# Kernel optimization log

Measured on AMD Instinct MI355X. Metric: run time of the kernel, lower is better.

Reference implementation:

```python
import jax, jax.numpy as jnp
import numpy as np

HIDDEN = 1024
B, S = 4, 2048


def setup_inputs() -> dict:
    key = jax.random.key(0)
    ks = jax.random.split(key, 9)
    scale = 1.0 / np.sqrt(HIDDEN)
    mk = lambda k: (jax.random.normal(k, (HIDDEN, HIDDEN), dtype=jnp.float32) * scale)
    return {
        "x": jax.random.normal(ks[0], (B, S, HIDDEN), dtype=jnp.float32),
        "Wq": mk(ks[1]), "bq": jnp.zeros((HIDDEN,), jnp.float32),
        "Wk": mk(ks[2]), "bk": jnp.zeros((HIDDEN,), jnp.float32),
        "Wv": mk(ks[3]), "bv": jnp.zeros((HIDDEN,), jnp.float32),
        "Wo": mk(ks[4]), "bo": jnp.zeros((HIDDEN,), jnp.float32),
    }


def reference(x, Wq, bq, Wk, bk, Wv, bv, Wo, bo):
    # Single-head attention over the full hidden dim (num_heads unused in source).
    # Linear(H,H): y = x @ W^T + b ; weights stored [out,in] torch-style.
    q = jnp.einsum("bsh,oh->bso", x, Wq) + bq  # [B,S,H]
    k = jnp.einsum("bsh,oh->bso", x, Wk) + bk
    v = jnp.einsum("bsh,oh->bso", x, Wv) + bv
    scores = jnp.einsum("bqh,bkh->bqk", q, k) / jnp.sqrt(jnp.float32(HIDDEN))
    attn = jax.nn.softmax(scores, axis=-1)  # dropout rate is 0.0 (eval-equivalent)
    ctx = jnp.einsum("bqk,bkh->bqh", attn, v)
    return jnp.einsum("bsh,oh->bso", ctx, Wo) + bo
```

## Files before the change

kernel.cpp:

```cpp
#include <hip/hip_runtime.h>

#define HID 1024
#define SEQ 2048
#define NB 4
#define BS 8192

typedef __attribute__((ext_vector_type(8))) short short8;
typedef __attribute__((ext_vector_type(8))) unsigned short ushort8;
typedef __attribute__((ext_vector_type(4))) float f32x4;

__device__ __forceinline__ float bf2f(unsigned short u) {
  unsigned int x = ((unsigned int)u) << 16;
  return __builtin_bit_cast(float, x);
}
__device__ __forceinline__ unsigned short f2bf(float f) {
  unsigned int x = __builtin_bit_cast(unsigned int, f);
  x = x + 0x7fffu + ((x >> 16) & 1u);
  return (unsigned short)(x >> 16);
}

#define GLOAD16(g, l)                                                          \
  __builtin_amdgcn_global_load_lds(                                            \
      (const __attribute__((address_space(1))) unsigned int*)(g),              \
      (__attribute__((address_space(3))) unsigned int*)(l), 16, 0, 0)

__global__ void cast_f32_to_bf16(const float* __restrict__ in,
                                 unsigned short* __restrict__ out, int n) {
  int i = (blockIdx.x * 256 + threadIdx.x) * 8;
  if (i >= n) return;
  f32x4 a = *(const f32x4*)(in + i);
  f32x4 b = *(const f32x4*)(in + i + 4);
  ushort8 o;
  o[0] = f2bf(a[0]); o[1] = f2bf(a[1]); o[2] = f2bf(a[2]); o[3] = f2bf(a[3]);
  o[4] = f2bf(b[0]); o[5] = f2bf(b[1]); o[6] = f2bf(b[2]); o[7] = f2bf(b[3]);
  *(ushort8*)(out + i) = o;
}

__global__ __launch_bounds__(256) void transpose_cast(
    const float* __restrict__ in, unsigned short* __restrict__ out) {
  __shared__ float t[32][33];
  const int bx = blockIdx.x * 32, by = blockIdx.y * 32;
  const int tx = threadIdx.x & 31, ty = threadIdx.x >> 5;
#pragma unroll
  for (int i = 0; i < 4; ++i)
    t[ty + i * 8][tx] = in[(by + ty + i * 8) * 1024 + bx + tx];
  __syncthreads();
#pragma unroll
  for (int i = 0; i < 4; ++i)
    out[(bx + ty + i * 8) * 1024 + by + tx] = f2bf(t[tx][ty + i * 8]);
}

__global__ __launch_bounds__(256) void bias_fuse(const float* __restrict__ Wo,
                                                 const float* __restrict__ bv,
                                                 const float* __restrict__ bo,
                                                 float* __restrict__ bp) {
  const int row = blockIdx.x * 4 + (threadIdx.x >> 6);
  const int lane = threadIdx.x & 63;
  float s = 0.f;
  for (int k = lane; k < 1024; k += 64) s += Wo[row * 1024 + k] * bv[k];
#pragma unroll
  for (int off = 32; off >= 1; off >>= 1) s += __shfl_xor(s, off, 64);
  if (lane == 0) bp[row] = s + bo[row];
}

template <int BN, int OUT_F32, int BIAS_MODE, int EPI>
__global__ __launch_bounds__(512, 2) void gemm2p(
    const unsigned short* __restrict__ A, const unsigned short* __restrict__ B,
    void* __restrict__ Cv, const float* __restrict__ bias,
    const float* __restrict__ bias2, float* __restrict__ Srow, int K, int lda,
    int ldb, int ldc, long long bsA, long long bsB, long long bsC,
    float alpha) {
  static_assert(BN == 256 || BN == 128, "BN");
  constexpr int WMW = (BN == 256) ? 2 : 4;
  constexpr int WNW = 8 / WMW;
  constexpr int MI = (256 / WMW) / 16;
  constexpr int GB = BN / 64;
  constexpr int WROWS = 256 / WMW;

  __shared__ unsigned short lA[2][256 * 64];
  __shared__ unsigned short lB[2][BN * 64];

  const int tid = threadIdx.x;
  const int lane = tid & 63, wid = tid >> 6;
  const int fr = lane & 15, fq = lane >> 4;
  const int wm = wid / WNW, wn = wid % WNW;

  const int nx = gridDim.x;
  const int nwg = nx * gridDim.y;
  int f = blockIdx.y * nx + blockIdx.x;
  f = (f & 7) * (nwg >> 3) + (f >> 3);
  const int bx = f % nx, by = f / nx;
  const int bz = blockIdx.z;

  const unsigned short* Ag = A + bz * bsA + (long long)by * 256 * lda;
  const unsigned short* Bg = B + bz * bsB + (long long)bx * BN * ldb;
  const int NT = K >> 6;

  const int srow = tid >> 3;
  const int gcol = 8 * ((tid & 7) ^ ((tid >> 3) & 7));
  const int ldst = wid * 512;

  auto stage = [&](int t) {
    const int b = t & 1;
#pragma unroll
    for (int c = 0; c < 4; ++c)
      GLOAD16(Ag + (long long)(c * 64 + srow) * lda + t * 64 + gcol,
              &lA[b][c * 4096 + ldst]);
#pragma unroll
    for (int c = 0; c < GB; ++c)
      GLOAD16(Bg + (long long)(c * 64 + srow) * ldb + t * 64 + gcol,
              &lB[b][c * 4096 + ldst]);
  };

  const int rxor = fr & 7;
  f32x4 acc[MI][4] = {};

  auto phase = [&](const unsigned short* pa, const unsigned short* pb,
                   int kk) {
    short8 av[MI], bw[4];
    const int slot = ((kk << 2) | fq) ^ rxor;
#pragma unroll
    for (int i = 0; i < MI; ++i)
      av[i] = *(const short8*)(pa + (wm * WROWS + i * 16 + fr) * 64 + slot * 8);
#pragma unroll
    for (int n = 0; n < 4; ++n)
      bw[n] = *(const short8*)(pb + (wn * 64 + n * 16 + fr) * 64 + slot * 8);
    asm volatile("s_waitcnt lgkmcnt(0)" ::: "memory");
    __builtin_amdgcn_sched_barrier(0);
    __builtin_amdgcn_s_setprio(1);
#pragma unroll
    for (int i = 0; i < MI; ++i)
#pragma unroll
      for (int n = 0; n < 4; ++n)
        acc[i][n] = __builtin_amdgcn_mfma_f32_16x16x32_bf16(av[i], bw[n],
                                                            acc[i][n], 0, 0, 0);
    __builtin_amdgcn_s_setprio(0);
  };

  stage(0);
  asm volatile("s_waitcnt vmcnt(0)" ::: "memory");
  __builtin_amdgcn_s_barrier();

  for (int t = 0; t < NT; ++t) {
    if (t + 1 < NT) stage(t + 1);
    const unsigned short* pa = lA[t & 1];
    const unsigned short* pb = lB[t & 1];
    phase(pa, pb, 0);
    phase(pa, pb, 1);
    asm volatile("s_waitcnt vmcnt(0)" ::: "memory");
    __builtin_amdgcn_s_barrier();
  }

  const long long cb0 = (long long)bz * bsC;
  float* sredf = (float*)lA;
#pragma unroll
  for (int i = 0; i < MI; ++i)
#pragma unroll
    for (int j = 0; j < 4; ++j) {
      const int row = wm * WROWS + i * 16 + fq * 4 + j;
      float inv = 1.0f;
      if (EPI == 2) inv = 1.0f / Srow[(long long)bz * SEQ + by * 256 + row];
      float rps = 0.0f;
#pragma unroll
      for (int n = 0; n < 4; ++n) {
        const int col = bx * BN + wn * 64 + n * 16 + fr;
        float v = acc[i][n][j] * alpha;
        if (EPI == 2) v *= inv;
        if (BIAS_MODE == 1) v += bias[col];
        if (BIAS_MODE == 3) v += (col < 1024) ? bias[col] : bias2[col - 1024];
        if (EPI == 1) { v = __expf(v); rps += v; }
        const long long idx = cb0 + (long long)(by * 256 + row) * ldc + col;
        if (OUT_F32)
          ((float*)Cv)[idx] = v;
        else
          ((unsigned short*)Cv)[idx] = f2bf(v);
      }
      if (EPI == 1) {
        rps += __shfl_xor(rps, 1, 64);
        rps += __shfl_xor(rps, 2, 64);
        rps += __shfl_xor(rps, 4, 64);
        rps += __shfl_xor(rps, 8, 64);
        if (fr == 0) sredf[row * WNW + wn] = rps;
      }
    }
  if (EPI == 1) {
    __syncthreads();
    if (tid < 256) {
      float s = 0.f;
#pragma unroll
      for (int w = 0; w < WNW; ++w) s += sredf[tid * WNW + w];
      atomicAdd(Srow + (long long)bz * SEQ + by * 256 + tid, s);
    }
  }
}

extern "C" void kernel_launch(void* const* d_in, const int* in_sizes, int n_in,
                              void* d_out, int out_size, void* d_ws,
                              size_t ws_size, hipStream_t stream) {
  (void)in_sizes; (void)n_in; (void)out_size; (void)ws_size;
  const float* x = (const float*)d_in[0];
  const float* Wq = (const float*)d_in[1];
  const float* bq = (const float*)d_in[2];
  const float* Wk = (const float*)d_in[3];
  const float* bk = (const float*)d_in[4];
  const float* Wv = (const float*)d_in[5];
  const float* bv = (const float*)d_in[6];
  const float* Wo = (const float*)d_in[7];
  const float* bo = (const float*)d_in[8];
  float* out = (float*)d_out;

  char* ws = (char*)d_ws;
  unsigned short* xbf  = (unsigned short*)(ws + 0);
  unsigned short* wqk  = (unsigned short*)(ws + 16777216);
  unsigned short* wobf = (unsigned short*)(ws + 20971520);
  unsigned short* wvT  = (unsigned short*)(ws + 23068672);
  unsigned short* wov  = (unsigned short*)(ws + 25165824);
  float*          bpr  = (float*)        (ws + 27262976);
  float*          Srow = (float*)        (ws + 28311552);
  unsigned short* VWoT = (unsigned short*)(ws + 33554432);
  unsigned short* QKb  = (unsigned short*)(ws + 50331648);
  unsigned short* P    = (unsigned short*)(ws + 83886080);

  cast_f32_to_bf16<<<4096, 256, 0, stream>>>(x, xbf, BS * HID);
  cast_f32_to_bf16<<<512, 256, 0, stream>>>(Wq, wqk, HID * HID);
  cast_f32_to_bf16<<<512, 256, 0, stream>>>(Wk, wqk + HID * HID, HID * HID);
  cast_f32_to_bf16<<<512, 256, 0, stream>>>(Wo, wobf, HID * HID);
  transpose_cast<<<dim3(32, 32), 256, 0, stream>>>(Wv, wvT);
  bias_fuse<<<256, 256, 0, stream>>>(Wo, bv, bo, bpr);
  hipMemsetAsync(Srow, 0, NB * SEQ * sizeof(float), stream);

  gemm2p<128, 0, 0, 0><<<dim3(8, 4, 1), 512, 0, stream>>>(
      wobf, wvT, wov, nullptr, nullptr, nullptr, HID, HID, HID, HID, 0, 0, 0,
      1.0f);
  gemm2p<128, 0, 0, 0><<<dim3(64, 4, 1), 512, 0, stream>>>(
      wov, xbf, VWoT, nullptr, nullptr, nullptr, HID, HID, HID, BS, 0, 0, 0,
      1.0f);
  gemm2p<256, 0, 3, 0><<<dim3(8, 32, 1), 512, 0, stream>>>(
      xbf, wqk, QKb, bq, bk, nullptr, HID, HID, HID, 2048, 0, 0, 0, 1.0f);
  gemm2p<256, 0, 0, 1><<<dim3(8, 8, NB), 512, 0, stream>>>(
      QKb, QKb + 1024, P, nullptr, nullptr, Srow, HID, 2048, 2048, SEQ,
      (long long)SEQ * 2048, (long long)SEQ * 2048, (long long)SEQ * SEQ,
      0.03125f);
  gemm2p<128, 1, 1, 2><<<dim3(8, 8, NB), 512, 0, stream>>>(
      P, VWoT, out, bpr, nullptr, Srow, SEQ, SEQ, BS, HID,
      (long long)SEQ * SEQ, (long long)SEQ, (long long)SEQ * HID, 1.0f);
}
```

Before: 215.4 us.

## Add smaller-tile gemm_s kernel for attention score and PV GEMMs

Adds a separate GEMM kernel that uses 256x128 tiles, a K-step of 32 and a smaller LDS footprint, with launch bounds allowing 4 blocks per CU. It is used for the QK^T+exp kernel and the P@VWo kernel. The goal is higher occupancy and more workgroups for these small-batch GEMMs, so the GPU is better filled and latency is better hidden. The epilogue features move out of gemm2p into the new kernel. The trade-off is a shorter pipeline per iteration and more barriers per unit of K.

```diff
diff --git a/kernel.cpp b/kernel.cpp
--- a/kernel.cpp
+++ b/kernel.cpp
@@ -63,13 +63,12 @@
   if (lane == 0) bp[row] = s + bo[row];
 }
 
-template <int BN, int OUT_F32, int BIAS_MODE, int EPI>
+template <int BN, int OUT_F32, int BIAS_MODE>
 __global__ __launch_bounds__(512, 2) void gemm2p(
     const unsigned short* __restrict__ A, const unsigned short* __restrict__ B,
     void* __restrict__ Cv, const float* __restrict__ bias,
-    const float* __restrict__ bias2, float* __restrict__ Srow, int K, int lda,
-    int ldb, int ldc, long long bsA, long long bsB, long long bsC,
-    float alpha) {
+    const float* __restrict__ bias2, int K, int lda, int ldb, int ldc,
+    long long bsA, long long bsB, long long bsC, float alpha) {
   static_assert(BN == 256 || BN == 128, "BN");
   constexpr int WMW = (BN == 256) ? 2 : 4;
   constexpr int WNW = 8 / WMW;
@@ -152,23 +151,115 @@
   }
 
   const long long cb0 = (long long)bz * bsC;
-  float* sredf = (float*)lA;
 #pragma unroll
   for (int i = 0; i < MI; ++i)
 #pragma unroll
     for (int j = 0; j < 4; ++j) {
       const int row = wm * WROWS + i * 16 + fq * 4 + j;
+#pragma unroll
+      for (int n = 0; n < 4; ++n) {
+        const int col = bx * BN + wn * 64 + n * 16 + fr;
+        float v = acc[i][n][j] * alpha;
+        if (BIAS_MODE == 1) v += bias[col];
+        if (BIAS_MODE == 3) v += (col < 1024) ? bias[col] : bias2[col - 1024];
+        const long long idx = cb0 + (long long)(by * 256 + row) * ldc + col;
+        if (OUT_F32)
+          ((float*)Cv)[idx] = v;
+        else
+          ((unsigned short*)Cv)[idx] = f2bf(v);
+      }
+    }
+}
+
+template <int OUT_F32, int BIAS_MODE, int EPI>
+__global__ __launch_bounds__(512, 4) void gemm_s(
+    const unsigned short* __restrict__ A, const unsigned short* __restrict__ B,
+    void* __restrict__ Cv, const float* __restrict__ bias,
+    float* __restrict__ Srow, int K, int lda, int ldb, int ldc, long long bsA,
+    long long bsB, long long bsC, float alpha) {
+  __shared__ unsigned short lA[2][256 * 32];
+  __shared__ unsigned short lB[2][128 * 32];
+
+  const int tid = threadIdx.x;
+  const int lane = tid & 63, wid = tid >> 6;
+  const int fr = lane & 15, fq = lane >> 4;
+  const int wm = wid >> 1, wn = wid & 1;
+
+  const int nx = gridDim.x;
+  const int nwg = nx * gridDim.y;
+  int f = blockIdx.y * nx + blockIdx.x;
+  f = (f & 7) * (nwg >> 3) + (f >> 3);
+  const int bx = f % nx, by = f / nx;
+  const int bz = blockIdx.z;
+
+  const unsigned short* Ag = A + bz * bsA + (long long)by * 256 * lda;
+  const unsigned short* Bg = B + bz * bsB + (long long)bx * 128 * ldb;
+  const int NT = K >> 5;
+
+  const int srow = tid >> 2;
+  const int scol = 8 * ((tid & 3) ^ ((tid >> 3) & 3));
+  const int ldst = wid * 512;
+
+  auto stage = [&](int t) {
+    const int b = t & 1;
+    GLOAD16(Ag + (long long)srow * lda + t * 32 + scol, &lA[b][ldst]);
+    GLOAD16(Ag + (long long)(128 + srow) * lda + t * 32 + scol,
+            &lA[b][4096 + ldst]);
+    GLOAD16(Bg + (long long)srow * ldb + t * 32 + scol, &lB[b][ldst]);
+  };
+
+  const int xm = ((fr >> 1) & 3) << 3;
+
+  f32x4 acc[4][4] = {};
+
+  stage(0);
+  asm volatile("s_waitcnt vmcnt(0)" ::: "memory");
+  __builtin_amdgcn_s_barrier();
+
+  for (int t = 0; t < NT; ++t) {
+    if (t + 1 < NT) stage(t + 1);
+    const unsigned short* pa = lA[t & 1];
+    const unsigned short* pb = lB[t & 1];
+    short8 av[4], bw[4];
+#pragma unroll
+    for (int i = 0; i < 4; ++i)
+      av[i] = *(const short8*)(pa +
+                               (((wm * 64 + i * 16 + fr) * 32 + fq * 8) ^ xm));
+#pragma unroll
+    for (int n = 0; n < 4; ++n)
+      bw[n] = *(const short8*)(pb +
+                               (((wn * 64 + n * 16 + fr) * 32 + fq * 8) ^ xm));
+    asm volatile("s_waitcnt lgkmcnt(0)" ::: "memory");
+    __builtin_amdgcn_sched_barrier(0);
+    __builtin_amdgcn_s_setprio(1);
+#pragma unroll
+    for (int i = 0; i < 4; ++i)
+#pragma unroll
+      for (int n = 0; n < 4; ++n)
+        acc[i][n] = __builtin_amdgcn_mfma_f32_16x16x32_bf16(av[i], bw[n],
+                                                            acc[i][n], 0, 0, 0);
+    __builtin_amdgcn_s_setprio(0);
+    asm volatile("s_waitcnt vmcnt(0)" ::: "memory");
+    __builtin_amdgcn_s_barrier();
+  }
+
+  const long long cb0 = (long long)bz * bsC;
+  float* sredf = (float*)lA;
+#pragma unroll
+  for (int i = 0; i < 4; ++i)
+#pragma unroll
+    for (int j = 0; j < 4; ++j) {
+      const int row = wm * 64 + i * 16 + fq * 4 + j;
       float inv = 1.0f;
       if (EPI == 2) inv = 1.0f / Srow[(long long)bz * SEQ + by * 256 + row];
       float rps = 0.0f;
 #pragma unroll
       for (int n = 0; n < 4; ++n) {
-        const int col = bx * BN + wn * 64 + n * 16 + fr;
+        const int col = bx * 128 + wn * 64 + n * 16 + fr;
         float v = acc[i][n][j] * alpha;
+        if (EPI == 1) { v = __expf(v); rps += v; }
         if (EPI == 2) v *= inv;
         if (BIAS_MODE == 1) v += bias[col];
-        if (BIAS_MODE == 3) v += (col < 1024) ? bias[col] : bias2[col - 1024];
-        if (EPI == 1) { v = __expf(v); rps += v; }
         const long long idx = cb0 + (long long)(by * 256 + row) * ldc + col;
         if (OUT_F32)
           ((float*)Cv)[idx] = v;
@@ -180,16 +271,14 @@
         rps += __shfl_xor(rps, 2, 64);
         rps += __shfl_xor(rps, 4, 64);
         rps += __shfl_xor(rps, 8, 64);
-        if (fr == 0) sredf[row * WNW + wn] = rps;
+        if (fr == 0) sredf[row * 2 + wn] = rps;
       }
     }
   if (EPI == 1) {
     __syncthreads();
     if (tid < 256) {
-      float s = 0.f;
-#pragma unroll
-      for (int w = 0; w < WNW; ++w) s += sredf[tid * WNW + w];
-      atomicAdd(Srow + (long long)bz * SEQ + by * 256 + tid, s);
+      const float s2 = sredf[tid * 2] + sredf[tid * 2 + 1];
+      atomicAdd(Srow + (long long)bz * SEQ + by * 256 + tid, s2);
     }
   }
 }
@@ -229,19 +318,17 @@
   bias_fuse<<<256, 256, 0, stream>>>(Wo, bv, bo, bpr);
   hipMemsetAsync(Srow, 0, NB * SEQ * sizeof(float), stream);
 
-  gemm2p<128, 0, 0, 0><<<dim3(8, 4, 1), 512, 0, stream>>>(
-      wobf, wvT, wov, nullptr, nullptr, nullptr, HID, HID, HID, HID, 0, 0, 0,
-      1.0f);
-  gemm2p<128, 0, 0, 0><<<dim3(64, 4, 1), 512, 0, stream>>>(
-      wov, xbf, VWoT, nullptr, nullptr, nullptr, HID, HID, HID, BS, 0, 0, 0,
-      1.0f);
-  gemm2p<256, 0, 3, 0><<<dim3(8, 32, 1), 512, 0, stream>>>(
-      xbf, wqk, QKb, bq, bk, nullptr, HID, HID, HID, 2048, 0, 0, 0, 1.0f);
-  gemm2p<256, 0, 0, 1><<<dim3(8, 8, NB), 512, 0, stream>>>(
-      QKb, QKb + 1024, P, nullptr, nullptr, Srow, HID, 2048, 2048, SEQ,
+  gemm2p<128, 0, 0><<<dim3(8, 4, 1), 512, 0, stream>>>(
+      wobf, wvT, wov, nullptr, nullptr, HID, HID, HID, HID, 0, 0, 0, 1.0f);
+  gemm2p<128, 0, 0><<<dim3(64, 4, 1), 512, 0, stream>>>(
+      wov, xbf, VWoT, nullptr, nullptr, HID, HID, HID, BS, 0, 0, 0, 1.0f);
+  gemm2p<256, 0, 3><<<dim3(8, 32, 1), 512, 0, stream>>>(
+      xbf, wqk, QKb, bq, bk, HID, HID, HID, 2048, 0, 0, 0, 1.0f);
+  gemm_s<0, 0, 1><<<dim3(16, 8, NB), 512, 0, stream>>>(
+      QKb, QKb + 1024, P, nullptr, Srow, HID, 2048, 2048, SEQ,
       (long long)SEQ * 2048, (long long)SEQ * 2048, (long long)SEQ * SEQ,
       0.03125f);
-  gemm2p<128, 1, 1, 2><<<dim3(8, 8, NB), 512, 0, stream>>>(
-      P, VWoT, out, bpr, nullptr, Srow, SEQ, SEQ, BS, HID,
-      (long long)SEQ * SEQ, (long long)SEQ, (long long)SEQ * HID, 1.0f);
-}
+  gemm_s<1, 1, 2><<<dim3(8, 8, NB), 512, 0, stream>>>(
+      P, VWoT, out, bpr, Srow, SEQ, SEQ, BS, HID, (long long)SEQ * SEQ,
+      (long long)SEQ, (long long)SEQ * HID, 1.0f);
+}
```

After: 224.0 us. 4.0% more time.
